# Performance work log

Hardware: AMD Instinct MI355X
Metric: run time of the kernel (lower is better)

## Reference

```python
import jax, jax.numpy as jnp
import numpy as np

RANK = 8
ALPHA = 8.0 / RANK  # module stores alpha/rank


def setup_inputs() -> dict:
    key = jax.random.key(0)
    k1, k2, k3, k4, k5 = jax.random.split(key, 5)
    M, N = 4096, 4096          # out_features, in_features
    T = 8192                   # flattened batch*seq tokens
    x = jax.random.normal(k1, (T, N), dtype=jnp.float32)
    W = jax.random.normal(k2, (M, N), dtype=jnp.float32) * 0.02
    b = jax.random.normal(k3, (M,), dtype=jnp.float32) * 0.02
    A = jax.random.normal(k4, (M, RANK), dtype=jnp.float32) * 0.01
    B = jax.random.normal(k5, (N, RANK), dtype=jnp.float32) * 0.01
    return {"x": x, "W": W, "b": b, "A": A, "B": B}


def reference(x, W, b, A, B):
    # Faithful to the torch module: delta_W = alpha * (A @ B.T) is materialized
    # [M, N], then out = linear(x) + F.linear(x, delta_W).
    delta_W = ALPHA * (A @ B.T)                 # [M, N]
    return x @ W.T + b + x @ delta_W.T          # [T, M]
```

## Files before the change

kernel.cpp:

```cpp
#include <hip/hip_runtime.h>
#include <cstdint>
#include <cstddef>


#define T_DIM 8192
#define M_DIM 4096
#define N_DIM 4096
#define RANK  8

typedef _Float16 f16x8 __attribute__((ext_vector_type(8)));
typedef float    f32x4 __attribute__((ext_vector_type(4)));

#define CAST_BLOCKS 16384
__global__ __launch_bounds__(256)
void prep_all(const float* __restrict__ x, const float* __restrict__ W,
              const float* __restrict__ A, const float* __restrict__ B,
              _Float16* __restrict__ Xh, _Float16* __restrict__ Wh) {
    const int bid = blockIdx.x;
    if (bid < CAST_BLOCKS) {
        size_t i = ((size_t)bid * 256 + threadIdx.x) * 8;
        f32x4 v0 = *(const f32x4*)(x + i);
        f32x4 v1 = *(const f32x4*)(x + i + 4);
        f16x8 o;
#pragma unroll
        for (int k = 0; k < 4; ++k) { o[k] = (_Float16)v0[k]; o[4 + k] = (_Float16)v1[k]; }
        *(f16x8*)(Xh + i) = o;
    } else {
        const size_t c = (size_t)(bid - CAST_BLOCKS) * 256 + threadIdx.x;
        const int m  = (int)(c >> 9);
        const int n0 = (int)(c & 511) << 3;
        f32x4 a0 = *(const f32x4*)(A + (size_t)m * RANK);
        f32x4 a1 = *(const f32x4*)(A + (size_t)m * RANK + 4);
        const float* wp = W + (size_t)m * N_DIM + n0;
        f32x4 w0 = *(const f32x4*)wp;
        f32x4 w1 = *(const f32x4*)(wp + 4);
        f16x8 o;
#pragma unroll
        for (int k = 0; k < 8; ++k) {
            const float* Bn = B + (size_t)(n0 + k) * RANK;
            f32x4 b0 = *(const f32x4*)Bn;
            f32x4 b1 = *(const f32x4*)(Bn + 4);
            float d = a0[0]*b0[0] + a0[1]*b0[1] + a0[2]*b0[2] + a0[3]*b0[3]
                    + a1[0]*b1[0] + a1[1]*b1[1] + a1[2]*b1[2] + a1[3]*b1[3];
            float wv = (k < 4) ? w0[k] : w1[k - 4];
            o[k] = (_Float16)(wv + d);
        }
        *(f16x8*)(Wh + (size_t)m * N_DIM + n0) = o;
    }
}

__device__ static inline void gld16(const _Float16* g, _Float16* l) {
    __builtin_amdgcn_global_load_lds(
        (const __attribute__((address_space(1))) unsigned int*)g,
        (__attribute__((address_space(3))) unsigned int*)l, 16, 0, 0);
}

__global__ __launch_bounds__(512, 2)
void gemm256(const _Float16* __restrict__ Xh, const _Float16* __restrict__ Wh,
             const float* __restrict__ bias, float* __restrict__ out) {
    __shared__ __align__(16) _Float16 lA[2][256 * 64];
    __shared__ __align__(16) _Float16 lB[2][256 * 64];

    const int tid  = threadIdx.x;
    const int lane = tid & 63;
    const int fr   = lane & 15;
    const int fq   = lane >> 4;
    const int w    = tid >> 6;
    const int wr   = w >> 2;
    const int wcn  = w & 3;

    const size_t rowX0 = (size_t)blockIdx.y * 256;
    const size_t rowW0 = (size_t)blockIdx.x * 256;

    const int srow = tid >> 3;
    const int scol = ((tid & 7) * 8) ^ ((srow & 7) * 8);
    const _Float16* sA = Xh + (rowX0 + srow) * N_DIM + scol;
    const _Float16* sBp[4];
#pragma unroll
    for (int cb = 0; cb < 4; ++cb) {
        const int p = cb * 64 + srow;
        const int wrow = ((p >> 5) & 3) * 64 + ((p >> 7) & 1) * 32 + (p & 31);
        sBp[cb] = Wh + (rowW0 + wrow) * N_DIM + scol;
    }

    const int kc0 = (fq * 8) ^ ((fr & 7) * 8);

    f32x4 acc[8][4] = {};
    f16x8 af[4][2], bf[4][2];

#define STAGE_A(b, rb, kt) gld16(sA + (size_t)(rb) * N_DIM + (kt) * 64, \
                                 &lA[b][(rb) * 64 + tid * 8])
#define STAGE_B(b, cb, kt) gld16(sBp[cb] + (size_t)(kt) * 64, \
                                 &lB[b][(cb) * 4096 + tid * 8])

#define LDA(b, qm) do { _Pragma("unroll") \
    for (int ii = 0; ii < 4; ++ii) { \
        const int ro_ = (wr * 128 + (qm) * 64 + ii * 16 + fr) * 64; \
        af[ii][0] = *(const f16x8*)&lA[b][ro_ + kc0]; \
        af[ii][1] = *(const f16x8*)&lA[b][ro_ + (kc0 ^ 32)]; } } while (0)

#define LDB(b, qn) do { _Pragma("unroll") \
    for (int jj = 0; jj < 2; ++jj) { \
        const int ro_ = ((qn) * 128 + wcn * 32 + jj * 16 + fr) * 64; \
        bf[(qn) * 2 + jj][0] = *(const f16x8*)&lB[b][ro_ + kc0]; \
        bf[(qn) * 2 + jj][1] = *(const f16x8*)&lB[b][ro_ + (kc0 ^ 32)]; } } while (0)

#define MMA(qm, qn) do { __builtin_amdgcn_s_setprio(1); \
    _Pragma("unroll") for (int ii = 0; ii < 4; ++ii) \
    _Pragma("unroll") for (int jj = 0; jj < 2; ++jj) { \
        acc[(qm)*4+ii][(qn)*2+jj] = __builtin_amdgcn_mfma_f32_16x16x32_f16( \
            af[ii][0], bf[(qn)*2+jj][0], acc[(qm)*4+ii][(qn)*2+jj], 0, 0, 0); \
        acc[(qm)*4+ii][(qn)*2+jj] = __builtin_amdgcn_mfma_f32_16x16x32_f16( \
            af[ii][1], bf[(qn)*2+jj][1], acc[(qm)*4+ii][(qn)*2+jj], 0, 0, 0); } \
    __builtin_amdgcn_s_setprio(0); \
    __builtin_amdgcn_sched_barrier(0); } while (0)

#define BAR asm volatile("s_barrier" ::: "memory")
#define VW4 asm volatile("s_waitcnt vmcnt(4)" ::: "memory")
#define VW0 asm volatile("s_waitcnt vmcnt(0)" ::: "memory")

    STAGE_A(0, 0, 0);  STAGE_A(0, 64, 0);  STAGE_A(0, 128, 0);  STAGE_A(0, 192, 0);
    STAGE_B(0, 0, 0);  STAGE_B(0, 1, 0);   STAGE_B(0, 2, 0);    STAGE_B(0, 3, 0);
    STAGE_A(1, 0, 1);  STAGE_A(1, 128, 1); STAGE_B(1, 0, 1);    STAGE_B(1, 1, 1);
    VW4; BAR;

#pragma unroll 1
    for (int n = 0; n < 31; ++n) {
        const int ko  = 2 * n + 1;
        const int ke2 = 2 * n + 2;
        const int ko2 = 2 * n + 3;
        STAGE_A(1, 64, ko); STAGE_A(1, 192, ko); STAGE_B(1, 2, ko); STAGE_B(1, 3, ko);
        LDA(0, 0); LDB(0, 0); LDB(0, 1);
        MMA(0, 0); MMA(0, 1);
        BAR;
        STAGE_A(0, 0, ke2); STAGE_A(0, 128, ke2); STAGE_B(0, 0, ke2); STAGE_B(0, 1, ke2);
        LDA(0, 1);
        MMA(1, 0); MMA(1, 1);
        VW4; BAR;
        STAGE_A(0, 64, ke2); STAGE_A(0, 192, ke2); STAGE_B(0, 2, ke2); STAGE_B(0, 3, ke2);
        LDA(1, 0); LDB(1, 0); LDB(1, 1);
        MMA(0, 0); MMA(0, 1);
        BAR;
        STAGE_A(1, 0, ko2); STAGE_A(1, 128, ko2); STAGE_B(1, 0, ko2); STAGE_B(1, 1, ko2);
        LDA(1, 1);
        MMA(1, 0); MMA(1, 1);
        VW4; BAR;
    }

    STAGE_A(1, 64, 63); STAGE_A(1, 192, 63); STAGE_B(1, 2, 63); STAGE_B(1, 3, 63);
    LDA(0, 0); LDB(0, 0); LDB(0, 1);
    MMA(0, 0); MMA(0, 1);
    BAR;
    LDA(0, 1);
    MMA(1, 0); MMA(1, 1);
    VW0; BAR;
    LDA(1, 0); LDB(1, 0); LDB(1, 1);
    MMA(0, 0); MMA(0, 1);
    LDA(1, 1);
    MMA(1, 0); MMA(1, 1);

    const int crow0 = (int)rowX0 + wr * 64;
    const int ccol0 = (int)rowW0 + wcn * 64;
    (void)crow0; (void)ccol0;
    {
        const int crow = (int)rowX0 + wr * 128;
        const int ccol = (int)rowW0 + wcn * 64;
        float bv[4];
#pragma unroll
        for (int j = 0; j < 4; ++j) bv[j] = bias[ccol + j * 16 + fr];
#pragma unroll
        for (int i = 0; i < 8; ++i) {
#pragma unroll
            for (int r = 0; r < 4; ++r) {
                const size_t row = (size_t)(crow + i * 16 + fq * 4 + r);
#pragma unroll
                for (int j = 0; j < 4; ++j)
                    out[row * M_DIM + ccol + j * 16 + fr] = acc[i][j][r] + bv[j];
            }
        }
    }
#undef STAGE_A
#undef STAGE_B
#undef LDA
#undef LDB
#undef MMA
#undef BAR
#undef VW4
#undef VW0
}

extern "C" void kernel_launch(void* const* d_in, const int* in_sizes, int n_in,
                              void* d_out, int out_size, void* d_ws, size_t ws_size,
                              hipStream_t stream) {
    const float* x = (const float*)d_in[0];
    const float* W = (const float*)d_in[1];
    const float* b = (const float*)d_in[2];
    const float* A = (const float*)d_in[3];
    const float* B = (const float*)d_in[4];
    float* out = (float*)d_out;

    _Float16* Wh = (_Float16*)d_ws;
    _Float16* Xh = (_Float16*)((char*)d_ws + (size_t)M_DIM * N_DIM * 2);

    prep_all<<<CAST_BLOCKS + (M_DIM * N_DIM / 8) / 256, 256, 0, stream>>>(
        x, W, A, B, Xh, Wh);

    dim3 grid(M_DIM / 256, T_DIM / 256);
    gemm256<<<grid, dim3(512, 1, 1), 0, stream>>>(Xh, Wh, b, out);
}
```

Before: 575.3 us.

## Split GEMM main loop into finer interleaved stage/compute phases with deeper prefetch

Restructures the double-buffered GEMM main loop so that each MMA quadrant becomes its own phase. Global-to-LDS staging for the next tile is spread across those phases instead of issued in large bursts, and the vmcnt wait moves from 4 to 6 so more loads stay in flight. Each MMA block now starts with an s_barrier and an lgkmcnt(0) wait, and another barrier follows it, to keep the wavefronts in lockstep. The aim is smoother overlap of memory traffic with matrix-core work, at the cost of many more workgroup barriers per iteration.

```diff
diff --git a/kernel.cpp b/kernel.cpp
--- a/kernel.cpp
+++ b/kernel.cpp
@@ -105,7 +105,10 @@
         bf[(qn) * 2 + jj][0] = *(const f16x8*)&lB[b][ro_ + kc0]; \
         bf[(qn) * 2 + jj][1] = *(const f16x8*)&lB[b][ro_ + (kc0 ^ 32)]; } } while (0)
 
-#define MMA(qm, qn) do { __builtin_amdgcn_s_setprio(1); \
+#define MMA(qm, qn) do { \
+    asm volatile("s_barrier" ::: "memory"); \
+    asm volatile("s_waitcnt lgkmcnt(0)" ::: "memory"); \
+    __builtin_amdgcn_s_setprio(1); \
     _Pragma("unroll") for (int ii = 0; ii < 4; ++ii) \
     _Pragma("unroll") for (int jj = 0; jj < 2; ++jj) { \
         acc[(qm)*4+ii][(qn)*2+jj] = __builtin_amdgcn_mfma_f32_16x16x32_f16( \
@@ -116,52 +119,61 @@
     __builtin_amdgcn_sched_barrier(0); } while (0)
 
 #define BAR asm volatile("s_barrier" ::: "memory")
-#define VW4 asm volatile("s_waitcnt vmcnt(4)" ::: "memory")
+#define VW6 asm volatile("s_waitcnt vmcnt(6)" ::: "memory")
 #define VW0 asm volatile("s_waitcnt vmcnt(0)" ::: "memory")
 
     STAGE_A(0, 0, 0);  STAGE_A(0, 64, 0);  STAGE_A(0, 128, 0);  STAGE_A(0, 192, 0);
     STAGE_B(0, 0, 0);  STAGE_B(0, 1, 0);   STAGE_B(0, 2, 0);    STAGE_B(0, 3, 0);
-    STAGE_A(1, 0, 1);  STAGE_A(1, 128, 1); STAGE_B(1, 0, 1);    STAGE_B(1, 1, 1);
-    VW4; BAR;
+    STAGE_A(1, 0, 1);  STAGE_A(1, 128, 1);
+    STAGE_B(1, 0, 1);  STAGE_B(1, 1, 1);
+    STAGE_A(1, 64, 1); STAGE_A(1, 192, 1);
+    VW6; BAR;
 
 #pragma unroll 1
     for (int n = 0; n < 31; ++n) {
         const int ko  = 2 * n + 1;
         const int ke2 = 2 * n + 2;
         const int ko2 = 2 * n + 3;
-        STAGE_A(1, 64, ko); STAGE_A(1, 192, ko); STAGE_B(1, 2, ko); STAGE_B(1, 3, ko);
-        LDA(0, 0); LDB(0, 0); LDB(0, 1);
-        MMA(0, 0); MMA(0, 1);
-        BAR;
-        STAGE_A(0, 0, ke2); STAGE_A(0, 128, ke2); STAGE_B(0, 0, ke2); STAGE_B(0, 1, ke2);
+        LDA(0, 0); LDB(0, 0);
+        STAGE_B(1, 2, ko); STAGE_B(1, 3, ko);
+        MMA(0, 0); BAR;
+        LDB(0, 1);
+        STAGE_A(0, 0, ke2); STAGE_A(0, 128, ke2);
+        MMA(0, 1); BAR;
         LDA(0, 1);
-        MMA(1, 0); MMA(1, 1);
-        VW4; BAR;
-        STAGE_A(0, 64, ke2); STAGE_A(0, 192, ke2); STAGE_B(0, 2, ke2); STAGE_B(0, 3, ke2);
-        LDA(1, 0); LDB(1, 0); LDB(1, 1);
-        MMA(0, 0); MMA(0, 1);
-        BAR;
-        STAGE_A(1, 0, ko2); STAGE_A(1, 128, ko2); STAGE_B(1, 0, ko2); STAGE_B(1, 1, ko2);
+        STAGE_B(0, 0, ke2); STAGE_B(0, 1, ke2);
+        MMA(1, 0); BAR;
+        STAGE_B(0, 2, ke2); STAGE_B(0, 3, ke2);
+        MMA(1, 1); VW6; BAR;
+        LDA(1, 0); LDB(1, 0);
+        STAGE_A(0, 64, ke2); STAGE_A(0, 192, ke2);
+        MMA(0, 0); BAR;
+        LDB(1, 1);
+        STAGE_A(1, 0, ko2); STAGE_A(1, 128, ko2);
+        MMA(0, 1); BAR;
         LDA(1, 1);
-        MMA(1, 0); MMA(1, 1);
-        VW4; BAR;
-    }
-
-    STAGE_A(1, 64, 63); STAGE_A(1, 192, 63); STAGE_B(1, 2, 63); STAGE_B(1, 3, 63);
-    LDA(0, 0); LDB(0, 0); LDB(0, 1);
-    MMA(0, 0); MMA(0, 1);
-    BAR;
+        STAGE_B(1, 0, ko2); STAGE_B(1, 1, ko2);
+        MMA(1, 0); BAR;
+        STAGE_A(1, 64, ko2); STAGE_A(1, 192, ko2);
+        MMA(1, 1); VW6; BAR;
+    }
+
+    LDA(0, 0); LDB(0, 0);
+    STAGE_B(1, 2, 63); STAGE_B(1, 3, 63);
+    MMA(0, 0); BAR;
+    LDB(0, 1);
+    MMA(0, 1); BAR;
     LDA(0, 1);
-    MMA(1, 0); MMA(1, 1);
-    VW0; BAR;
-    LDA(1, 0); LDB(1, 0); LDB(1, 1);
-    MMA(0, 0); MMA(0, 1);
+    MMA(1, 0); BAR;
+    MMA(1, 1); VW0; BAR;
+    LDA(1, 0); LDB(1, 0);
+    MMA(0, 0); BAR;
+    LDB(1, 1);
+    MMA(0, 1); BAR;
     LDA(1, 1);
-    MMA(1, 0); MMA(1, 1);
-
-    const int crow0 = (int)rowX0 + wr * 64;
-    const int ccol0 = (int)rowW0 + wcn * 64;
-    (void)crow0; (void)ccol0;
+    MMA(1, 0); BAR;
+    MMA(1, 1);
+
     {
         const int crow = (int)rowX0 + wr * 128;
         const int ccol = (int)rowW0 + wcn * 64;
@@ -185,7 +197,7 @@
 #undef LDB
 #undef MMA
 #undef BAR
-#undef VW4
+#undef VW6
 #undef VW0
 }
 
```

Result: faster. 556.5 us (-3.3%).

## Restructure GEMM main loop with register-rotated fragments and per-K-tile staging

Applied to the files above, without the earlier changes.

Rewrites the 256x256 GEMM inner loop so each wave keeps all four B fragments resident and streams A fragments through a rotating set of named registers. Global-to-LDS staging is now issued per whole K-tile (all A rows, then all B rows) instead of half-tiles, and LDS reads are interleaved between MFMA groups with extra barriers and priority hints. Global addressing switches from 64-bit pointers to 32-bit int offsets. The aim is better overlap of LDS reads with MFMA work and less address arithmetic. In exchange it adds more barriers and a full vmcnt(0) wait per tile, which may expose load latency.

```diff
diff --git a/kernel.cpp b/kernel.cpp
--- a/kernel.cpp
+++ b/kernel.cpp
@@ -74,94 +74,131 @@
 
     const int srow = tid >> 3;
     const int scol = ((tid & 7) * 8) ^ ((srow & 7) * 8);
-    const _Float16* sA = Xh + (rowX0 + srow) * N_DIM + scol;
-    const _Float16* sBp[4];
-#pragma unroll
-    for (int cb = 0; cb < 4; ++cb) {
-        const int p = cb * 64 + srow;
-        const int wrow = ((p >> 5) & 3) * 64 + ((p >> 7) & 1) * 32 + (p & 31);
-        sBp[cb] = Wh + (rowW0 + wrow) * N_DIM + scol;
+    const int aofs = (int)((rowX0 + srow) * N_DIM) + scol;
+    int wofs0, wofs1, wofs2, wofs3;
+    {
+        int t[4];
+#pragma unroll
+        for (int cb = 0; cb < 4; ++cb) {
+            const int p = cb * 64 + srow;
+            const int wrow = ((p >> 5) & 3) * 64 + ((p >> 7) & 1) * 32 + (p & 31);
+            t[cb] = (int)((rowW0 + wrow) * N_DIM) + scol;
+        }
+        wofs0 = t[0]; wofs1 = t[1]; wofs2 = t[2]; wofs3 = t[3];
     }
 
     const int kc0 = (fq * 8) ^ ((fr & 7) * 8);
 
     f32x4 acc[8][4] = {};
-    f16x8 af[4][2], bf[4][2];
-
-#define STAGE_A(b, rb, kt) gld16(sA + (size_t)(rb) * N_DIM + (kt) * 64, \
+    f16x8 a0_0, a0_1, a1_0, a1_1, a2_0, a2_1, a3_0, a3_1, a4_0, a4_1;
+    f16x8 b0_0, b0_1, b1_0, b1_1, b2_0, b2_1, b3_0, b3_1;
+
+#define STAGE_A(b, rb, kt) gld16(Xh + aofs + (rb) * N_DIM + (kt) * 64, \
                                  &lA[b][(rb) * 64 + tid * 8])
-#define STAGE_B(b, cb, kt) gld16(sBp[cb] + (size_t)(kt) * 64, \
-                                 &lB[b][(cb) * 4096 + tid * 8])
-
-#define LDA(b, qm) do { _Pragma("unroll") \
-    for (int ii = 0; ii < 4; ++ii) { \
-        const int ro_ = (wr * 128 + (qm) * 64 + ii * 16 + fr) * 64; \
-        af[ii][0] = *(const f16x8*)&lA[b][ro_ + kc0]; \
-        af[ii][1] = *(const f16x8*)&lA[b][ro_ + (kc0 ^ 32)]; } } while (0)
-
-#define LDB(b, qn) do { _Pragma("unroll") \
-    for (int jj = 0; jj < 2; ++jj) { \
-        const int ro_ = ((qn) * 128 + wcn * 32 + jj * 16 + fr) * 64; \
-        bf[(qn) * 2 + jj][0] = *(const f16x8*)&lB[b][ro_ + kc0]; \
-        bf[(qn) * 2 + jj][1] = *(const f16x8*)&lB[b][ro_ + (kc0 ^ 32)]; } } while (0)
-
-#define MMA(qm, qn) do { __builtin_amdgcn_s_setprio(1); \
-    _Pragma("unroll") for (int ii = 0; ii < 4; ++ii) \
-    _Pragma("unroll") for (int jj = 0; jj < 2; ++jj) { \
-        acc[(qm)*4+ii][(qn)*2+jj] = __builtin_amdgcn_mfma_f32_16x16x32_f16( \
-            af[ii][0], bf[(qn)*2+jj][0], acc[(qm)*4+ii][(qn)*2+jj], 0, 0, 0); \
-        acc[(qm)*4+ii][(qn)*2+jj] = __builtin_amdgcn_mfma_f32_16x16x32_f16( \
-            af[ii][1], bf[(qn)*2+jj][1], acc[(qm)*4+ii][(qn)*2+jj], 0, 0, 0); } \
-    __builtin_amdgcn_s_setprio(0); \
-    __builtin_amdgcn_sched_barrier(0); } while (0)
-
-#define BAR asm volatile("s_barrier" ::: "memory")
-#define VW4 asm volatile("s_waitcnt vmcnt(4)" ::: "memory")
-#define VW0 asm volatile("s_waitcnt vmcnt(0)" ::: "memory")
-
-    STAGE_A(0, 0, 0);  STAGE_A(0, 64, 0);  STAGE_A(0, 128, 0);  STAGE_A(0, 192, 0);
-    STAGE_B(0, 0, 0);  STAGE_B(0, 1, 0);   STAGE_B(0, 2, 0);    STAGE_B(0, 3, 0);
-    STAGE_A(1, 0, 1);  STAGE_A(1, 128, 1); STAGE_B(1, 0, 1);    STAGE_B(1, 1, 1);
-    VW4; BAR;
+#define STAGE_B0(b, kt) gld16(Wh + wofs0 + (kt) * 64, &lB[b][tid * 8])
+#define STAGE_B1(b, kt) gld16(Wh + wofs1 + (kt) * 64, &lB[b][4096 + tid * 8])
+#define STAGE_B2(b, kt) gld16(Wh + wofs2 + (kt) * 64, &lB[b][8192 + tid * 8])
+#define STAGE_B3(b, kt) gld16(Wh + wofs3 + (kt) * 64, &lB[b][12288 + tid * 8])
+
+#define RDA(d0, d1, b, i) do { \
+    const int ro_ = (wr * 128 + (i) * 16 + fr) * 64; \
+    d0 = *(const f16x8*)&lA[b][ro_ + kc0]; \
+    d1 = *(const f16x8*)&lA[b][ro_ + (kc0 ^ 32)]; } while (0)
+#define RDB(d0, d1, b, j) do { \
+    const int ro_ = (((j) >> 1) * 128 + wcn * 32 + ((j) & 1) * 16 + fr) * 64; \
+    d0 = *(const f16x8*)&lB[b][ro_ + kc0]; \
+    d1 = *(const f16x8*)&lB[b][ro_ + (kc0 ^ 32)]; } while (0)
+
+#define MF(a, b, c) __builtin_amdgcn_mfma_f32_16x16x32_f16(a, b, c, 0, 0, 0)
+
+#define S8(x0, x1, I) do { \
+    acc[I][0] = MF(x0, b0_0, acc[I][0]); acc[I][0] = MF(x1, b0_1, acc[I][0]); \
+    acc[I][1] = MF(x0, b1_0, acc[I][1]); acc[I][1] = MF(x1, b1_1, acc[I][1]); \
+    acc[I][2] = MF(x0, b2_0, acc[I][2]); acc[I][2] = MF(x1, b2_1, acc[I][2]); \
+    acc[I][3] = MF(x0, b3_0, acc[I][3]); acc[I][3] = MF(x1, b3_1, acc[I][3]); } while (0)
+
+#define T8(y0, y1, J, p40, p41, p50, p51, p60, p61, p70, p71) do { \
+    acc[4][J] = MF(p40, y0, acc[4][J]); acc[4][J] = MF(p41, y1, acc[4][J]); \
+    acc[5][J] = MF(p50, y0, acc[5][J]); acc[5][J] = MF(p51, y1, acc[5][J]); \
+    acc[6][J] = MF(p60, y0, acc[6][J]); acc[6][J] = MF(p61, y1, acc[6][J]); \
+    acc[7][J] = MF(p70, y0, acc[7][J]); acc[7][J] = MF(p71, y1, acc[7][J]); } while (0)
+
+#define T8E(y0, y1, J) T8(y0, y1, J, a3_0, a3_1, a0_0, a0_1, a1_0, a1_1, a2_0, a2_1)
+#define T8O(y0, y1, J) T8(y0, y1, J, a3_0, a3_1, a4_0, a4_1, a1_0, a1_1, a2_0, a2_1)
+
+#define BAR   asm volatile("s_barrier" ::: "memory")
+#define VW0   asm volatile("s_waitcnt vmcnt(0)" ::: "memory")
+#define PRIO1 __builtin_amdgcn_s_setprio(1)
+#define PRIO0 __builtin_amdgcn_s_setprio(0)
+#define SB    __builtin_amdgcn_sched_barrier(0)
+
+    STAGE_A(0, 0, 0); STAGE_A(0, 64, 0); STAGE_A(0, 128, 0); STAGE_A(0, 192, 0);
+    STAGE_B0(0, 0); STAGE_B1(0, 0); STAGE_B2(0, 0); STAGE_B3(0, 0);
+    VW0; BAR;
+    RDA(a0_0, a0_1, 0, 0);
+    RDB(b0_0, b0_1, 0, 0); RDB(b1_0, b1_1, 0, 1);
+    RDB(b2_0, b2_1, 0, 2); RDB(b3_0, b3_1, 0, 3);
 
 #pragma unroll 1
     for (int n = 0; n < 31; ++n) {
         const int ko  = 2 * n + 1;
         const int ke2 = 2 * n + 2;
-        const int ko2 = 2 * n + 3;
-        STAGE_A(1, 64, ko); STAGE_A(1, 192, ko); STAGE_B(1, 2, ko); STAGE_B(1, 3, ko);
-        LDA(0, 0); LDB(0, 0); LDB(0, 1);
-        MMA(0, 0); MMA(0, 1);
-        BAR;
-        STAGE_A(0, 0, ke2); STAGE_A(0, 128, ke2); STAGE_B(0, 0, ke2); STAGE_B(0, 1, ke2);
-        LDA(0, 1);
-        MMA(1, 0); MMA(1, 1);
-        VW4; BAR;
-        STAGE_A(0, 64, ke2); STAGE_A(0, 192, ke2); STAGE_B(0, 2, ke2); STAGE_B(0, 3, ke2);
-        LDA(1, 0); LDB(1, 0); LDB(1, 1);
-        MMA(0, 0); MMA(0, 1);
-        BAR;
-        STAGE_A(1, 0, ko2); STAGE_A(1, 128, ko2); STAGE_B(1, 0, ko2); STAGE_B(1, 1, ko2);
-        LDA(1, 1);
-        MMA(1, 0); MMA(1, 1);
-        VW4; BAR;
-    }
-
-    STAGE_A(1, 64, 63); STAGE_A(1, 192, 63); STAGE_B(1, 2, 63); STAGE_B(1, 3, 63);
-    LDA(0, 0); LDB(0, 0); LDB(0, 1);
-    MMA(0, 0); MMA(0, 1);
-    BAR;
-    LDA(0, 1);
-    MMA(1, 0); MMA(1, 1);
-    VW0; BAR;
-    LDA(1, 0); LDB(1, 0); LDB(1, 1);
-    MMA(0, 0); MMA(0, 1);
-    LDA(1, 1);
-    MMA(1, 0); MMA(1, 1);
-
-    const int crow0 = (int)rowX0 + wr * 64;
-    const int ccol0 = (int)rowW0 + wcn * 64;
-    (void)crow0; (void)ccol0;
+        RDA(a1_0, a1_1, 0, 1); RDA(a2_0, a2_1, 0, 2); RDA(a3_0, a3_1, 0, 4);
+        STAGE_A(1, 0, ko); STAGE_A(1, 64, ko); STAGE_A(1, 128, ko); STAGE_A(1, 192, ko);
+        BAR; PRIO1; S8(a0_0, a0_1, 0); S8(a1_0, a1_1, 1); PRIO0; SB; BAR;
+        RDA(a4_0, a4_1, 0, 3); RDA(a0_0, a0_1, 0, 5); RDA(a1_0, a1_1, 0, 6);
+        STAGE_B0(1, ko); STAGE_B1(1, ko); STAGE_B2(1, ko); STAGE_B3(1, ko);
+        BAR; PRIO1; S8(a2_0, a2_1, 2);
+        RDA(a2_0, a2_1, 0, 7);
+        S8(a4_0, a4_1, 3); PRIO0; SB; BAR;
+        PRIO1; T8E(b0_0, b0_1, 0); T8E(b1_0, b1_1, 1); PRIO0; SB; VW0; BAR;
+        RDB(b0_0, b0_1, 1, 0); RDB(b1_0, b1_1, 1, 1); RDA(a4_0, a4_1, 1, 0);
+        BAR; PRIO1; T8E(b2_0, b2_1, 2);
+        RDB(b2_0, b2_1, 1, 2);
+        T8E(b3_0, b3_1, 3); PRIO0;
+        RDB(b3_0, b3_1, 1, 3);
+        SB; BAR;
+        RDA(a1_0, a1_1, 1, 1); RDA(a2_0, a2_1, 1, 2); RDA(a3_0, a3_1, 1, 4);
+        STAGE_A(0, 0, ke2); STAGE_A(0, 64, ke2); STAGE_A(0, 128, ke2); STAGE_A(0, 192, ke2);
+        BAR; PRIO1; S8(a4_0, a4_1, 0); S8(a1_0, a1_1, 1); PRIO0; SB; BAR;
+        RDA(a0_0, a0_1, 1, 3); RDA(a4_0, a4_1, 1, 5); RDA(a1_0, a1_1, 1, 6);
+        STAGE_B0(0, ke2); STAGE_B1(0, ke2); STAGE_B2(0, ke2); STAGE_B3(0, ke2);
+        BAR; PRIO1; S8(a2_0, a2_1, 2);
+        RDA(a2_0, a2_1, 1, 7);
+        S8(a0_0, a0_1, 3); PRIO0; SB; BAR;
+        PRIO1; T8O(b0_0, b0_1, 0); T8O(b1_0, b1_1, 1); PRIO0; SB; VW0; BAR;
+        RDB(b0_0, b0_1, 0, 0); RDB(b1_0, b1_1, 0, 1); RDA(a0_0, a0_1, 0, 0);
+        BAR; PRIO1; T8O(b2_0, b2_1, 2);
+        RDB(b2_0, b2_1, 0, 2);
+        T8O(b3_0, b3_1, 3); PRIO0;
+        RDB(b3_0, b3_1, 0, 3);
+        SB; BAR;
+    }
+
+    RDA(a1_0, a1_1, 0, 1); RDA(a2_0, a2_1, 0, 2); RDA(a3_0, a3_1, 0, 4);
+    STAGE_A(1, 0, 63); STAGE_A(1, 64, 63); STAGE_A(1, 128, 63); STAGE_A(1, 192, 63);
+    BAR; PRIO1; S8(a0_0, a0_1, 0); S8(a1_0, a1_1, 1); PRIO0; SB; BAR;
+    RDA(a4_0, a4_1, 0, 3); RDA(a0_0, a0_1, 0, 5); RDA(a1_0, a1_1, 0, 6);
+    STAGE_B0(1, 63); STAGE_B1(1, 63); STAGE_B2(1, 63); STAGE_B3(1, 63);
+    BAR; PRIO1; S8(a2_0, a2_1, 2);
+    RDA(a2_0, a2_1, 0, 7);
+    S8(a4_0, a4_1, 3); PRIO0; SB; BAR;
+    PRIO1; T8E(b0_0, b0_1, 0); T8E(b1_0, b1_1, 1); PRIO0; SB; VW0; BAR;
+    RDB(b0_0, b0_1, 1, 0); RDB(b1_0, b1_1, 1, 1); RDA(a4_0, a4_1, 1, 0);
+    BAR; PRIO1; T8E(b2_0, b2_1, 2);
+    RDB(b2_0, b2_1, 1, 2);
+    T8E(b3_0, b3_1, 3); PRIO0;
+    RDB(b3_0, b3_1, 1, 3);
+    SB; BAR;
+    RDA(a1_0, a1_1, 1, 1); RDA(a2_0, a2_1, 1, 2); RDA(a3_0, a3_1, 1, 4);
+    BAR; PRIO1; S8(a4_0, a4_1, 0); S8(a1_0, a1_1, 1); PRIO0; SB; BAR;
+    RDA(a0_0, a0_1, 1, 3); RDA(a4_0, a4_1, 1, 5); RDA(a1_0, a1_1, 1, 6);
+    BAR; PRIO1; S8(a2_0, a2_1, 2);
+    RDA(a2_0, a2_1, 1, 7);
+    S8(a0_0, a0_1, 3); PRIO0; SB; BAR;
+    PRIO1; T8O(b0_0, b0_1, 0); T8O(b1_0, b1_1, 1);
+    T8O(b2_0, b2_1, 2); T8O(b3_0, b3_1, 3); PRIO0;
+
     {
         const int crow = (int)rowX0 + wr * 128;
         const int ccol = (int)rowW0 + wcn * 64;
@@ -180,13 +217,22 @@
         }
     }
 #undef STAGE_A
-#undef STAGE_B
-#undef LDA
-#undef LDB
-#undef MMA
+#undef STAGE_B0
+#undef STAGE_B1
+#undef STAGE_B2
+#undef STAGE_B3
+#undef RDA
+#undef RDB
+#undef MF
+#undef S8
+#undef T8
+#undef T8E
+#undef T8O
 #undef BAR
-#undef VW4
 #undef VW0
+#undef PRIO1
+#undef PRIO0
+#undef SB
 }
 
 extern "C" void kernel_launch(void* const* d_in, const int* in_sizes, int n_in,
```

Measured after the change: 558.7 us. -2.9%, faster.
